# Kernel optimization log

Measured on AMD Instinct MI355X. Metric: run time of the kernel, lower is better.

## Reference

```python
import jax, jax.numpy as jnp
import numpy as np

D_MODEL = 768
N_LAYER = 4
VOCAB = 50257
D_STATE = 16
D_CONV = 4
D_INNER = 2 * D_MODEL
DT_RANK = 48
B, L = 1, 2048


def setup_inputs() -> dict:
    key = jax.random.key(0)
    ks = jax.random.split(key, 12)
    n = lambda k, shape, s=0.02: jax.random.normal(k, shape, dtype=jnp.float32) * s
    return {
        "idx": jax.random.randint(ks[0], (B, L), 0, VOCAB, dtype=jnp.int32),
        "targets": jax.random.randint(ks[1], (B, L), 0, VOCAB, dtype=jnp.int32),
        "embedding": n(ks[2], (VOCAB, D_MODEL)),
        "norm_w": jnp.ones((N_LAYER, D_MODEL), jnp.float32),
        "in_proj_w": n(ks[3], (N_LAYER, 2 * D_INNER, D_MODEL)),
        "conv_w": n(ks[4], (N_LAYER, D_INNER, D_CONV), 0.1),
        "conv_b": jnp.zeros((N_LAYER, D_INNER), jnp.float32),
        "x_proj_w": n(ks[5], (N_LAYER, DT_RANK + 2 * D_STATE, D_INNER)),
        "dt_proj_w": n(ks[6], (N_LAYER, D_INNER, DT_RANK), 0.1),
        # bias so softplus(dt) lands in ~[0.01, 0.1] as in the official init
        "dt_proj_b": jax.random.uniform(ks[7], (N_LAYER, D_INNER), jnp.float32, -4.6, -2.3),
        # A_log = log(1..d_state), the standard S4D-real init
        "A_log": jnp.log(jnp.broadcast_to(jnp.arange(1, D_STATE + 1, dtype=jnp.float32), (N_LAYER, D_INNER, D_STATE))),
        "D_param": jnp.ones((N_LAYER, D_INNER), jnp.float32),
        "out_proj_w": n(ks[8], (N_LAYER, D_MODEL, D_INNER)),
        "norm_f_w": jnp.ones((D_MODEL,), jnp.float32),
    }


def rmsnorm(x, w, eps=1e-5):
    return x * jax.lax.rsqrt(jnp.mean(x * x, -1, keepdims=True) + eps) * w


def causal_conv1d(x, w, b):
    # x: (B,L,d_inner); w: (d_inner, K) depthwise causal conv
    K = w.shape[-1]
    Lx = x.shape[1]
    xp = jnp.pad(x, ((0, 0), (K - 1, 0), (0, 0)))
    y = b
    for k in range(K):
        y = y + xp[:, k:k + Lx, :] * w[:, k]
    return y


def selective_scan(x, dt, A, Bm, Cm, Dp):
    # x, dt: (B,L,d_inner); A: (d_inner,d_state); Bm, Cm: (B,L,d_state)
    bsz, _, d_in = x.shape

    def step(h, inp):
        x_t, dt_t, B_t, C_t = inp  # (B,d_in),(B,d_in),(B,s),(B,s)
        h = jnp.exp(dt_t[:, :, None] * A) * h + (dt_t * x_t)[:, :, None] * B_t[:, None, :]
        return h, jnp.einsum('bds,bs->bd', h, C_t)

    h0 = jnp.zeros((bsz, d_in, A.shape[-1]), x.dtype)
    _, ys = jax.lax.scan(step, h0, (x.swapaxes(0, 1), dt.swapaxes(0, 1), Bm.swapaxes(0, 1), Cm.swapaxes(0, 1)))
    return ys.swapaxes(0, 1) + x * Dp


def mamba_block(x, in_w, cw, cb, xpw, dtw, dtb, a_log, dp, ow):
    xz = x @ in_w.T  # (B,L,2*d_inner)
    xi, z = jnp.split(xz, 2, axis=-1)
    xi = jax.nn.silu(causal_conv1d(xi, cw, cb))
    xdbl = xi @ xpw.T  # (B,L,dt_rank+2*d_state)
    dt = xdbl[..., :DT_RANK]
    Bm = xdbl[..., DT_RANK:DT_RANK + D_STATE]
    Cm = xdbl[..., DT_RANK + D_STATE:]
    dt = jax.nn.softplus(dt @ dtw.T + dtb)
    A = -jnp.exp(a_log)
    y = selective_scan(xi, dt, A, Bm, Cm, dp)
    y = y * jax.nn.silu(z)
    return y @ ow.T


def reference(idx, targets, embedding, norm_w, in_proj_w, conv_w, conv_b, x_proj_w,
              dt_proj_w, dt_proj_b, A_log, D_param, out_proj_w, norm_f_w):
    x = embedding[idx]  # (B,L,D)
    for l in range(N_LAYER):
        x = x + mamba_block(rmsnorm(x, norm_w[l]), in_proj_w[l], conv_w[l], conv_b[l],
                            x_proj_w[l], dt_proj_w[l], dt_proj_b[l], A_log[l],
                            D_param[l], out_proj_w[l])
    x = rmsnorm(x, norm_f_w)
    logits = x @ embedding.T  # tied lm head, (B,L,V)
    # cross_entropy with ignore_index=-1
    logp = jax.nn.log_softmax(logits, axis=-1)
    mask = (targets >= 0).astype(logits.dtype)
    tgt = jnp.clip(targets, 0, VOCAB - 1)
    nll = -jnp.take_along_axis(logp, tgt[..., None], axis=-1)[..., 0]
    loss = jnp.sum(nll * mask) / jnp.maximum(jnp.sum(mask), 1.0)
    return (logits, loss)
```

## Files before the change

### kernel.cpp

```cpp
#include <hip/hip_runtime.h>
#include <stdint.h>


#define D_MODEL 768
#define N_LAYER 4
#define VOCAB 50257
#define D_STATE 16
#define D_INNER 1536
#define DT_RANK 48
#define LSEQ 2048
#define TCHUNK 64
#define NCHUNK 32

#define EMB_E 39321600L
#define W1E 2359296L
#define W2E 196608L
#define W3E 98304L
#define W4E 1179648L
#define PERL (W1E + W2E + W3E + W4E)
#define TOTCVT (EMB_E + 4 * PERL)

typedef unsigned short u16;
typedef __attribute__((ext_vector_type(8))) short short8;
typedef __attribute__((ext_vector_type(4))) float f32x4;

__device__ __forceinline__ u16 f2bf(float f) {
  unsigned int x = __float_as_uint(f);
  x += 0x7fffu + ((x >> 16) & 1u);
  return (u16)(x >> 16);
}
__device__ __forceinline__ float bf2f(u16 v) {
  return __uint_as_float(((unsigned int)v) << 16);
}
__device__ __forceinline__ void gl16(const void* g, void* l) {
  __builtin_amdgcn_global_load_lds((const __attribute__((address_space(1))) void*)g,
                                   (__attribute__((address_space(3))) void*)l, 16, 0, 0);
}

#define PIPELINE(NT)                                                          \
  STAGE(0, 0);                                                                \
  STAGE(32, 1);                                                               \
  {                                                                           \
    int cur = 0;                                                              \
    for (int t = 0; t < (NT); t++) {                                          \
      if (t + 1 < (NT)) { asm volatile("s_waitcnt vmcnt(4)" ::: "memory"); }  \
      else              { asm volatile("s_waitcnt vmcnt(0)" ::: "memory"); }  \
      asm volatile("s_barrier" ::: "memory");                                 \
      short8 af[4], bfr[4];                                                   \
      _Pragma("unroll")                                                       \
      for (int i = 0; i < 4; i++)                                             \
        af[i] = *(const short8*)(&lA[cur][(wm + i * 16 + fr) * 32 + kh]);     \
      _Pragma("unroll")                                                       \
      for (int j = 0; j < 4; j++)                                             \
        bfr[j] = *(const short8*)(&lB[cur][(wn + j * 16 + fr) * 32 + kh]);    \
      asm volatile("s_waitcnt lgkmcnt(0)" ::: "memory");                      \
      asm volatile("s_barrier" ::: "memory");                                 \
      if (t + 2 < (NT)) STAGE((t + 2) * 32, cur);                             \
      _Pragma("unroll")                                                       \
      for (int i = 0; i < 4; i++)                                             \
        _Pragma("unroll")                                                     \
        for (int j = 0; j < 4; j++)                                           \
          acc[i][j] = __builtin_amdgcn_mfma_f32_16x16x32_bf16(af[i], bfr[j],  \
                                                              acc[i][j], 0, 0, 0); \
      cur ^= 1;                                                               \
    }                                                                         \
  }

__global__ void k_convert_all(const float* __restrict__ emb, const float* __restrict__ in_w,
                              const float* __restrict__ xp_w, const float* __restrict__ dt_w,
                              const float* __restrict__ out_w, u16* __restrict__ dst) {
  long i = (long)blockIdx.x * 256 + threadIdx.x;
  float v;
  if (i < EMB_E) {
    long n = i / D_MODEL, k = i % D_MODEL;
    v = (n < VOCAB) ? emb[n * D_MODEL + k] : 0.0f;
  } else {
    long j = i - EMB_E;
    int l = (int)(j / PERL);
    long m = j % PERL;
    if (m < W1E) {
      v = in_w[(long)l * W1E + m];
    } else if (m < W1E + W2E) {
      long mm = m - W1E;
      long n = mm / D_INNER, k = mm % D_INNER;
      v = (n < 80) ? xp_w[(long)l * 80 * D_INNER + n * D_INNER + k] : 0.0f;
    } else if (m < W1E + W2E + W3E) {
      long mm = m - (W1E + W2E);
      long n = mm / 64, k = mm % 64;
      v = (k < DT_RANK) ? dt_w[(long)l * D_INNER * DT_RANK + n * DT_RANK + k] : 0.0f;
    } else {
      long mm = m - (W1E + W2E + W3E);
      v = out_w[(long)l * W4E + mm];
    }
  }
  dst[i] = f2bf(v);
}

__global__ void k_embed_rms(const int* __restrict__ idx, const float* __restrict__ emb,
                            const float* __restrict__ w, float* __restrict__ x,
                            u16* __restrict__ xnb) {
  int t = blockIdx.x, tid = threadIdx.x;
  __shared__ float red[256];
  const float* src = emb + (long)idx[t] * D_MODEL;
  float g[3];
  float s = 0.0f;
#pragma unroll
  for (int q = 0; q < 3; q++) {
    g[q] = src[tid + q * 256];
    s += g[q] * g[q];
  }
  red[tid] = s; __syncthreads();
  for (int o = 128; o > 0; o >>= 1) { if (tid < o) red[tid] += red[tid + o]; __syncthreads(); }
  float scale = rsqrtf(red[0] / (float)D_MODEL + 1e-5f);
#pragma unroll
  for (int q = 0; q < 3; q++) {
    int c = tid + q * 256;
    x[(long)t * D_MODEL + c] = g[q];
    xnb[(long)t * D_MODEL + c] = f2bf(g[q] * scale * w[c]);
  }
}

__global__ void k_rms_red(const float* __restrict__ part, const float* __restrict__ w,
                          float* __restrict__ x, u16* __restrict__ xnb) {
  int t = blockIdx.x, tid = threadIdx.x;
  __shared__ float red[256];
  float g[3];
  float s = 0.0f;
#pragma unroll
  for (int q = 0; q < 3; q++) {
    int c = tid + q * 256;
    long off = (long)t * D_MODEL + c;
    float v = x[off];
#pragma unroll
    for (int p = 0; p < 4; p++) v += part[(size_t)p * LSEQ * D_MODEL + off];
    g[q] = v;
    s += v * v;
  }
  red[tid] = s; __syncthreads();
  for (int o = 128; o > 0; o >>= 1) { if (tid < o) red[tid] += red[tid + o]; __syncthreads(); }
  float scale = rsqrtf(red[0] / (float)D_MODEL + 1e-5f);
#pragma unroll
  for (int q = 0; q < 3; q++) {
    int c = tid + q * 256;
    x[(long)t * D_MODEL + c] = g[q];
    xnb[(long)t * D_MODEL + c] = f2bf(g[q] * scale * w[c]);
  }
}

template<int EPI>
__global__ __launch_bounds__(256) void k_gemm2(
    const u16* __restrict__ A, const u16* __restrict__ W, void* __restrict__ Cv,
    const float* __restrict__ bias, int N, int K, int lda, int ldb, int ldc) {
  __shared__ u16 lA[2][128 * 32];
  __shared__ u16 lB[2][128 * 32];
  const int gx = gridDim.x, gy = gridDim.y;
  int id = blockIdx.x + gx * blockIdx.y;
  int q8 = (gx * gy) >> 3;
  int v = (id & 7) * q8 + (id >> 3);
  const int bx = v / gy, by = v % gy;
  const int brow = by * 128, bcol = bx * 128;
  const int tid = threadIdx.x, wid = tid >> 6, lane = tid & 63;
  const int wm = (wid >> 1) * 64, wn = (wid & 1) * 64;
  const int fr = lane & 15, fq = lane >> 4;
  const int kh = 8 * (fq ^ ((fr >> 1) & 3));
  const int srow = tid >> 2;
  const int lcol = (tid & 3) * 8;
  const int scol = 8 * ((tid & 3) ^ ((srow >> 1) & 3));
  const u16* ga0 = A + (size_t)(brow + srow) * lda + scol;
  const u16* ga1 = A + (size_t)(brow + srow + 64) * lda + scol;
  const u16* gb0 = W + (size_t)(bcol + srow) * ldb + scol;
  const u16* gb1 = W + (size_t)(bcol + srow + 64) * ldb + scol;
  const int lo = srow * 32 + lcol;

  f32x4 acc[4][4];
#pragma unroll
  for (int i = 0; i < 4; i++)
#pragma unroll
    for (int j = 0; j < 4; j++)
#pragma unroll
      for (int r = 0; r < 4; r++) acc[i][j][r] = 0.0f;

  auto STAGE = [&](int k0, int b) {
    gl16(ga0 + k0, &lA[b][lo]);
    gl16(ga1 + k0, &lA[b][lo + 2048]);
    gl16(gb0 + k0, &lB[b][lo]);
    gl16(gb1 + k0, &lB[b][lo + 2048]);
  };

  PIPELINE(K / 32);

#pragma unroll
  for (int i = 0; i < 4; i++)
#pragma unroll
    for (int j = 0; j < 4; j++) {
      int col = bcol + wn + j * 16 + fr;
      if (col < N) {
#pragma unroll
        for (int r = 0; r < 4; r++) {
          int row = brow + wm + i * 16 + fq * 4 + r;
          float val = acc[i][j][r];
          if (EPI == 1) {
            val += bias[col];
            val = (val > 20.0f) ? val : log1pf(__expf(val));
            ((float*)Cv)[(size_t)row * ldc + col] = val;
          } else {
            ((u16*)Cv)[(size_t)row * ldc + col] = f2bf(val);
          }
        }
      }
    }
}

__global__ __launch_bounds__(256) void k_gemm_part(
    const u16* __restrict__ A, const u16* __restrict__ W, float* __restrict__ Cp,
    int N, int Ks, int lda, int ldb, int ldc) {
  __shared__ u16 lA[2][128 * 32];
  __shared__ u16 lB[2][128 * 32];
  const int gx = gridDim.x, gy = gridDim.y;
  int id = blockIdx.x + gx * blockIdx.y;
  int q8 = (gx * gy) >> 3;
  int v = (id & 7) * q8 + (id >> 3);
  const int bx = v / gy, by = v % gy;
  const int brow = by * 128, bcol = bx * 128;
  const int koff = blockIdx.z * Ks;
  const int tid = threadIdx.x, wid = tid >> 6, lane = tid & 63;
  const int wm = (wid >> 1) * 64, wn = (wid & 1) * 64;
  const int fr = lane & 15, fq = lane >> 4;
  const int kh = 8 * (fq ^ ((fr >> 1) & 3));
  const int srow = tid >> 2;
  const int lcol = (tid & 3) * 8;
  const int scol = 8 * ((tid & 3) ^ ((srow >> 1) & 3));
  const u16* ga0 = A + (size_t)(brow + srow) * lda + koff + scol;
  const u16* ga1 = A + (size_t)(brow + srow + 64) * lda + koff + scol;
  const u16* gb0 = W + (size_t)(bcol + srow) * ldb + koff + scol;
  const u16* gb1 = W + (size_t)(bcol + srow + 64) * ldb + koff + scol;
  const int lo = srow * 32 + lcol;

  f32x4 acc[4][4];
#pragma unroll
  for (int i = 0; i < 4; i++)
#pragma unroll
    for (int j = 0; j < 4; j++)
#pragma unroll
      for (int r = 0; r < 4; r++) acc[i][j][r] = 0.0f;

  auto STAGE = [&](int k0, int b) {
    gl16(ga0 + k0, &lA[b][lo]);
    gl16(ga1 + k0, &lA[b][lo + 2048]);
    gl16(gb0 + k0, &lB[b][lo]);
    gl16(gb1 + k0, &lB[b][lo + 2048]);
  };

  PIPELINE(Ks / 32);

  float* Cz = Cp + (size_t)blockIdx.z * LSEQ * ldc;
#pragma unroll
  for (int i = 0; i < 4; i++)
#pragma unroll
    for (int j = 0; j < 4; j++) {
      int col = bcol + wn + j * 16 + fr;
      if (col < N) {
#pragma unroll
        for (int r = 0; r < 4; r++) {
          int row = brow + wm + i * 16 + fq * 4 + r;
          Cz[(size_t)row * ldc + col] = acc[i][j][r];
        }
      }
    }
}

__global__ __launch_bounds__(256, 2) void k_gemm_logits(
    const u16* __restrict__ A, const u16* __restrict__ W, float* __restrict__ C,
    float* __restrict__ part) {
  __shared__ u16 lA[2][256 * 32];
  __shared__ u16 lB[2][128 * 32];
  const int b = blockIdx.x;
  const int xcd = b & 7, slot = b >> 3;
  const int ct = xcd * 50 + (slot >> 3), rt = slot & 7;
  const int brow = rt * 256, bcol = ct * 128;
  const int tid = threadIdx.x, wid = tid >> 6, lane = tid & 63;
  const int wm = (wid >> 1) * 128, wn = (wid & 1) * 64;
  const int fr = lane & 15, fq = lane >> 4;
  const int kh = 8 * (fq ^ ((fr >> 1) & 3));
  const int srow = tid >> 2;
  const int lcol = (tid & 3) * 8;
  const int scol = 8 * ((tid & 3) ^ ((srow >> 1) & 3));
  const u16* ga = A + (size_t)(brow + srow) * D_MODEL + scol;
  const u16* gb = W + (size_t)(bcol + srow) * D_MODEL + scol;
  const int lo = srow * 32 + lcol;

  f32x4 acc[8][4];
#pragma unroll
  for (int i = 0; i < 8; i++)
#pragma unroll
    for (int j = 0; j < 4; j++)
#pragma unroll
      for (int r = 0; r < 4; r++) acc[i][j][r] = 0.0f;

  auto STAGE = [&](int k0, int bb) {
    gl16(ga + k0, &lA[bb][lo]);
    gl16(ga + (size_t)64 * D_MODEL + k0, &lA[bb][lo + 2048]);
    gl16(ga + (size_t)128 * D_MODEL + k0, &lA[bb][lo + 4096]);
    gl16(ga + (size_t)192 * D_MODEL + k0, &lA[bb][lo + 6144]);
    gl16(gb + k0, &lB[bb][lo]);
    gl16(gb + (size_t)64 * D_MODEL + k0, &lB[bb][lo + 2048]);
  };

  STAGE(0, 0);
  STAGE(32, 1);
  int cur = 0;
  const int NT = D_MODEL / 32;
  for (int t = 0; t < NT; t++) {
    if (t + 1 < NT) { asm volatile("s_waitcnt vmcnt(6)" ::: "memory"); }
    else            { asm volatile("s_waitcnt vmcnt(0)" ::: "memory"); }
    asm volatile("s_barrier" ::: "memory");
    short8 af[8], bfr[4];
#pragma unroll
    for (int i = 0; i < 8; i++)
      af[i] = *(const short8*)(&lA[cur][(wm + i * 16 + fr) * 32 + kh]);
#pragma unroll
    for (int j = 0; j < 4; j++)
      bfr[j] = *(const short8*)(&lB[cur][(wn + j * 16 + fr) * 32 + kh]);
    asm volatile("s_waitcnt lgkmcnt(0)" ::: "memory");
    asm volatile("s_barrier" ::: "memory");
    if (t + 2 < NT) STAGE((t + 2) * 32, cur);
    __builtin_amdgcn_s_setprio(1);
#pragma unroll
    for (int i = 0; i < 8; i++)
#pragma unroll
      for (int j = 0; j < 4; j++)
        acc[i][j] = __builtin_amdgcn_mfma_f32_16x16x32_bf16(af[i], bfr[j], acc[i][j], 0, 0, 0);
    __builtin_amdgcn_s_setprio(0);
    cur ^= 1;
  }

  float rs[32];
#pragma unroll
  for (int q = 0; q < 32; q++) rs[q] = 0.0f;
#pragma unroll
  for (int i = 0; i < 8; i++)
#pragma unroll
    for (int j = 0; j < 4; j++) {
      int col = bcol + wn + j * 16 + fr;
      if (col < VOCAB) {
#pragma unroll
        for (int r = 0; r < 4; r++) {
          int row = brow + wm + i * 16 + fq * 4 + r;
          float val = acc[i][j][r];
          C[(size_t)row * VOCAB + col] = val;
          rs[i * 4 + r] += __expf(val - 20.0f);
        }
      }
    }
#pragma unroll
  for (int q = 0; q < 32; q++) {
    float s = rs[q];
    s += __shfl_xor(s, 1); s += __shfl_xor(s, 2);
    s += __shfl_xor(s, 4); s += __shfl_xor(s, 8);
    rs[q] = s;
  }
  if (fr == 0) {
    int pc = ct * 2 + (wn >> 6);
#pragma unroll
    for (int i = 0; i < 8; i++)
#pragma unroll
      for (int r = 0; r < 4; r++) {
        int row = brow + wm + i * 16 + fq * 4 + r;
        part[(size_t)pc * LSEQ + row] = rs[i * 4 + r];
      }
  }
}

__global__ void k_conv_silu(const u16* __restrict__ xzb, const float* __restrict__ cw,
                            const float* __restrict__ cb, u16* __restrict__ xib) {
  int i = blockIdx.x * 256 + threadIdx.x;
  int t = i / (D_INNER / 8), d8 = (i % (D_INNER / 8)) * 8;
  float acc[8];
#pragma unroll
  for (int q = 0; q < 8; q++) acc[q] = cb[d8 + q];
#pragma unroll
  for (int k = 0; k < 4; k++) {
    int tt = t - 3 + k;
    if (tt >= 0) {
      short8 v = *(const short8*)(xzb + (long)tt * (2 * D_INNER) + d8);
#pragma unroll
      for (int q = 0; q < 8; q++) acc[q] += bf2f((u16)v[q]) * cw[(d8 + q) * 4 + k];
    }
  }
  short8 o;
#pragma unroll
  for (int q = 0; q < 8; q++) {
    float s = acc[q] / (1.0f + __expf(-acc[q]));
    o[q] = (short)f2bf(s);
  }
  *(short8*)(xib + (long)t * D_INNER + d8) = o;
}

__global__ void k_red_xd(const float* __restrict__ pxp, float* __restrict__ xdbl,
                         u16* __restrict__ dtp) {
  int i = blockIdx.x * 256 + threadIdx.x;
  int t = i >> 7, k = i & 127;
  if (k < 80) {
    float s = 0.0f;
#pragma unroll
    for (int p = 0; p < 8; p++) s += pxp[(size_t)p * LSEQ * 80 + (long)t * 80 + k];
    xdbl[(long)t * 80 + k] = s;
    if (k < DT_RANK) dtp[(long)t * 64 + k] = f2bf(s);
    else if (k < 64) dtp[(long)t * 64 + k] = 0;
  }
}

__global__ void k_scanA(const float* __restrict__ dt, const u16* __restrict__ xi,
                        const float* __restrict__ xdbl, const float* __restrict__ a_log,
                        float* __restrict__ aprod, float* __restrict__ hend) {
  int d = blockIdx.x * 256 + threadIdx.x;
  int c = blockIdx.y;
  float A[16], ap[16], h[16];
#pragma unroll
  for (int s = 0; s < 16; s++) { A[s] = -__expf(a_log[d * 16 + s]); ap[s] = 1.0f; h[s] = 0.0f; }
  int t0 = c * TCHUNK;
  for (int t = t0; t < t0 + TCHUNK; t++) {
    float dtv = dt[(long)t * D_INNER + d], xv = bf2f(xi[(long)t * D_INNER + d]);
    float dx = dtv * xv;
    const float* Bp = xdbl + (long)t * 80 + DT_RANK;
#pragma unroll
    for (int s = 0; s < 16; s++) {
      float a = __expf(dtv * A[s]);
      h[s] = a * h[s] + dx * Bp[s];
      ap[s] *= a;
    }
  }
  long base = ((long)c * D_INNER + d) * 16;
#pragma unroll
  for (int s = 0; s < 16; s++) { aprod[base + s] = ap[s]; hend[base + s] = h[s]; }
}

__global__ void k_scanB(const float* __restrict__ aprod, const float* __restrict__ hend,
                        float* __restrict__ hinit) {
  int i = blockIdx.x * 256 + threadIdx.x;
  float h = 0.0f;
  for (int c = 0; c < NCHUNK; c++) {
    long idx = (long)c * D_INNER * 16 + i;
    hinit[idx] = h;
    h = aprod[idx] * h + hend[idx];
  }
}

__global__ void k_scanC(const float* __restrict__ dt, const u16* __restrict__ xi,
                        const float* __restrict__ xdbl, const float* __restrict__ a_log,
                        const float* __restrict__ hinit, const float* __restrict__ Dp,
                        const u16* __restrict__ xzb, u16* __restrict__ yb) {
  int d = blockIdx.x * 256 + threadIdx.x;
  int c = blockIdx.y;
  float A[16], h[16];
  long hb = (long)c * D_INNER * 16 + (long)d * 16;
#pragma unroll
  for (int s = 0; s < 16; s++) { A[s] = -__expf(a_log[d * 16 + s]); h[s] = hinit[hb + s]; }
  float Dv = Dp[d];
  int t0 = c * TCHUNK;
  for (int t = t0; t < t0 + TCHUNK; t++) {
    float dtv = dt[(long)t * D_INNER + d], xv = bf2f(xi[(long)t * D_INNER + d]);
    float dx = dtv * xv;
    const float* Bp = xdbl + (long)t * 80 + DT_RANK;
    const float* Cp = Bp + D_STATE;
    float o = xv * Dv;
#pragma unroll
    for (int s = 0; s < 16; s++) {
      float a = __expf(dtv * A[s]);
      h[s] = a * h[s] + dx * Bp[s];
      o += h[s] * Cp[s];
    }
    float z = bf2f(xzb[(long)t * (2 * D_INNER) + D_INNER + d]);
    yb[(long)t * D_INNER + d] = f2bf(o * (z / (1.0f + __expf(-z))));
  }
}

__global__ void k_lse_final(const float* __restrict__ part, const float* __restrict__ logits,
                            const int* __restrict__ tgt, float* __restrict__ nll,
                            float* __restrict__ msk) {
  int t = blockIdx.x * 256 + threadIdx.x;
  float s = 0.0f;
  for (int p = 0; p < 800; p++) s += part[(size_t)p * LSEQ + t];
  float lse = 20.0f + __logf(s);
  int tg = tgt[t];
  float mk = tg >= 0 ? 1.0f : 0.0f;
  int tc = tg < 0 ? 0 : (tg > VOCAB - 1 ? VOCAB - 1 : tg);
  nll[t] = (lse - logits[(size_t)t * VOCAB + tc]) * mk;
  msk[t] = mk;
}

__global__ void k_loss(const float* __restrict__ nll, const float* __restrict__ msk,
                       float* __restrict__ out) {
  int tid = threadIdx.x;
  __shared__ float r1[256], r2[256];
  float a = 0.0f, b = 0.0f;
  for (int i = tid; i < LSEQ; i += 256) { a += nll[i]; b += msk[i]; }
  r1[tid] = a; r2[tid] = b; __syncthreads();
  for (int o = 128; o > 0; o >>= 1) {
    if (tid < o) { r1[tid] += r1[tid + o]; r2[tid] += r2[tid + o]; }
    __syncthreads();
  }
  if (tid == 0) out[0] = r1[0] / fmaxf(r2[0], 1.0f);
}

extern "C" void kernel_launch(void* const* d_in, const int* in_sizes, int n_in,
                              void* d_out, int out_size, void* d_ws, size_t ws_size,
                              hipStream_t stream) {
  const int*   idx    = (const int*)d_in[0];
  const int*   tgt    = (const int*)d_in[1];
  const float* emb    = (const float*)d_in[2];
  const float* norm_w = (const float*)d_in[3];
  const float* in_w   = (const float*)d_in[4];
  const float* conv_w = (const float*)d_in[5];
  const float* conv_b = (const float*)d_in[6];
  const float* xp_w   = (const float*)d_in[7];
  const float* dt_w   = (const float*)d_in[8];
  const float* dt_b   = (const float*)d_in[9];
  const float* a_log  = (const float*)d_in[10];
  const float* d_par  = (const float*)d_in[11];
  const float* out_w  = (const float*)d_in[12];
  const float* normf  = (const float*)d_in[13];

  float* logits = (float*)d_out;
  float* loss   = logits + (size_t)LSEQ * VOCAB;

  char* base = (char*)d_ws;
  size_t off = 0;
  auto alloc = [&](size_t bytes) -> char* {
    char* r = base + off;
    off = (off + bytes + 255) & ~(size_t)255;
    return r;
  };
  u16*   wcat = (u16*)  alloc((size_t)TOTCVT * 2);
  float* x    = (float*)alloc((size_t)LSEQ * D_MODEL * 4);
  u16*   xnb  = (u16*)  alloc((size_t)LSEQ * D_MODEL * 2);
  u16*   xzb  = (u16*)  alloc((size_t)LSEQ * 2 * D_INNER * 2);
  u16*   xib  = (u16*)  alloc((size_t)LSEQ * D_INNER * 2);
  float* xdbl = (float*)alloc((size_t)LSEQ * 80 * 4);
  u16*   dtp  = (u16*)  alloc((size_t)LSEQ * 64 * 2);
  float* dtl  = (float*)alloc((size_t)LSEQ * D_INNER * 4);
  u16*   yb   = (u16*)  alloc((size_t)LSEQ * D_INNER * 2);
  float* pxp  = (float*)alloc((size_t)8 * LSEQ * 80 * 4);
  float* pop  = (float*)alloc((size_t)4 * LSEQ * D_MODEL * 4);
  float* apr  = (float*)alloc((size_t)NCHUNK * D_INNER * 16 * 4);
  float* hen  = (float*)alloc((size_t)NCHUNK * D_INNER * 16 * 4);
  float* hin  = (float*)alloc((size_t)NCHUNK * D_INNER * 16 * 4);
  float* nll  = (float*)alloc((size_t)LSEQ * 4);
  float* msk  = (float*)alloc((size_t)LSEQ * 4);
  float* part = pop;
  (void)ws_size; (void)in_sizes; (void)n_in; (void)out_size;

  const u16* embb = wcat;

  k_convert_all<<<(unsigned)(TOTCVT / 256), 256, 0, stream>>>(emb, in_w, xp_w, dt_w, out_w, wcat);
  k_embed_rms<<<LSEQ, 256, 0, stream>>>(idx, emb, norm_w, x, xnb);

  for (int l = 0; l < N_LAYER; l++) {
    const u16* w1 = wcat + EMB_E + (long)l * PERL;
    const u16* w2 = w1 + W1E;
    const u16* w3 = w2 + W2E;
    const u16* w4 = w3 + W3E;

    k_gemm2<2><<<dim3(24, 16), 256, 0, stream>>>(
        xnb, w1, xzb, nullptr, 2 * D_INNER, D_MODEL, D_MODEL, D_MODEL, 2 * D_INNER);

    k_conv_silu<<<(LSEQ * D_INNER / 8) / 256, 256, 0, stream>>>(
        xzb, conv_w + (long)l * D_INNER * 4, conv_b + l * D_INNER, xib);

    k_gemm_part<<<dim3(1, 16, 8), 256, 0, stream>>>(
        xib, w2, pxp, 80, D_INNER / 8, D_INNER, D_INNER, 80);
    k_red_xd<<<(LSEQ * 128) / 256, 256, 0, stream>>>(pxp, xdbl, dtp);

    k_gemm2<1><<<dim3(12, 16), 256, 0, stream>>>(
        dtp, w3, dtl, dt_b + l * D_INNER, D_INNER, 64, 64, 64, D_INNER);

    const float* al = a_log + (long)l * D_INNER * D_STATE;
    k_scanA<<<dim3(D_INNER / 256, NCHUNK), 256, 0, stream>>>(dtl, xib, xdbl, al, apr, hen);
    k_scanB<<<(D_INNER * 16) / 256, 256, 0, stream>>>(apr, hen, hin);
    k_scanC<<<dim3(D_INNER / 256, NCHUNK), 256, 0, stream>>>(
        dtl, xib, xdbl, al, hin, d_par + l * D_INNER, xzb, yb);

    k_gemm_part<<<dim3(6, 16, 4), 256, 0, stream>>>(
        yb, w4, pop, D_MODEL, D_INNER / 4, D_INNER, D_INNER, D_MODEL);

    const float* wn = (l < N_LAYER - 1) ? (norm_w + (l + 1) * D_MODEL) : normf;
    k_rms_red<<<LSEQ, 256, 0, stream>>>(pop, wn, x, xnb);
  }

  k_gemm_logits<<<400 * 8, 256, 0, stream>>>(xnb, embb, logits, part);
  k_lse_final<<<LSEQ / 256, 256, 0, stream>>>(part, logits, tgt, nll, msk);
  k_loss<<<1, 256, 0, stream>>>(nll, msk, loss);
}
```

Measured before the change: 1.171 ms.

## Triple-buffer GEMM pipelines, vectorize weight conversion, and retune split-K and logits occupancy

Deepens the GEMM shared-memory pipeline from two to three stages and raises wave priority around the MFMA block, so more loads are in flight and compute is favoured over issue. The bf16 weight conversion kernel now handles four elements per thread with a vector store. The x_proj split-K factor doubles to 16, logits stores become nontemporal, and the logits kernel's launch bounds now request 3 blocks per SM instead of 2. Partial-sum buffers are merged into one pool. The extra LDS per GEMM block and the tighter register budget for logits may reduce occupancy or cause spills.

```diff
diff --git a/kernel.cpp b/kernel.cpp
--- a/kernel.cpp
+++ b/kernel.cpp
@@ -23,6 +23,7 @@
 typedef unsigned short u16;
 typedef __attribute__((ext_vector_type(8))) short short8;
 typedef __attribute__((ext_vector_type(4))) float f32x4;
+typedef __attribute__((ext_vector_type(4))) unsigned short us4;
 
 __device__ __forceinline__ u16 f2bf(float f) {
   unsigned int x = __float_as_uint(f);
@@ -37,14 +38,17 @@
                                    (__attribute__((address_space(3))) void*)l, 16, 0, 0);
 }
 
-#define PIPELINE(NT)                                                          \
+#define PIPELINE3(NT)                                                         \
   STAGE(0, 0);                                                                \
-  STAGE(32, 1);                                                               \
+  if ((NT) > 1) STAGE(32, 1);                                                 \
+  if ((NT) > 2) STAGE(64, 2);                                                 \
   {                                                                           \
     int cur = 0;                                                              \
     for (int t = 0; t < (NT); t++) {                                          \
-      if (t + 1 < (NT)) { asm volatile("s_waitcnt vmcnt(4)" ::: "memory"); }  \
-      else              { asm volatile("s_waitcnt vmcnt(0)" ::: "memory"); }  \
+      int rem = (NT) - 1 - t;                                                 \
+      if (rem >= 2)      { asm volatile("s_waitcnt vmcnt(8)" ::: "memory"); } \
+      else if (rem == 1) { asm volatile("s_waitcnt vmcnt(4)" ::: "memory"); } \
+      else               { asm volatile("s_waitcnt vmcnt(0)" ::: "memory"); } \
       asm volatile("s_barrier" ::: "memory");                                 \
       short8 af[4], bfr[4];                                                   \
       _Pragma("unroll")                                                       \
@@ -55,45 +59,54 @@
         bfr[j] = *(const short8*)(&lB[cur][(wn + j * 16 + fr) * 32 + kh]);    \
       asm volatile("s_waitcnt lgkmcnt(0)" ::: "memory");                      \
       asm volatile("s_barrier" ::: "memory");                                 \
-      if (t + 2 < (NT)) STAGE((t + 2) * 32, cur);                             \
+      if (t + 3 < (NT)) STAGE((t + 3) * 32, cur);                             \
+      __builtin_amdgcn_s_setprio(1);                                          \
       _Pragma("unroll")                                                       \
       for (int i = 0; i < 4; i++)                                             \
         _Pragma("unroll")                                                     \
         for (int j = 0; j < 4; j++)                                           \
           acc[i][j] = __builtin_amdgcn_mfma_f32_16x16x32_bf16(af[i], bfr[j],  \
                                                               acc[i][j], 0, 0, 0); \
-      cur ^= 1;                                                               \
+      __builtin_amdgcn_s_setprio(0);                                          \
+      cur = (cur == 2) ? 0 : cur + 1;                                         \
     }                                                                         \
   }
 
 __global__ void k_convert_all(const float* __restrict__ emb, const float* __restrict__ in_w,
                               const float* __restrict__ xp_w, const float* __restrict__ dt_w,
                               const float* __restrict__ out_w, u16* __restrict__ dst) {
-  long i = (long)blockIdx.x * 256 + threadIdx.x;
-  float v;
-  if (i < EMB_E) {
-    long n = i / D_MODEL, k = i % D_MODEL;
-    v = (n < VOCAB) ? emb[n * D_MODEL + k] : 0.0f;
-  } else {
-    long j = i - EMB_E;
-    int l = (int)(j / PERL);
-    long m = j % PERL;
-    if (m < W1E) {
-      v = in_w[(long)l * W1E + m];
-    } else if (m < W1E + W2E) {
-      long mm = m - W1E;
-      long n = mm / D_INNER, k = mm % D_INNER;
-      v = (n < 80) ? xp_w[(long)l * 80 * D_INNER + n * D_INNER + k] : 0.0f;
-    } else if (m < W1E + W2E + W3E) {
-      long mm = m - (W1E + W2E);
-      long n = mm / 64, k = mm % 64;
-      v = (k < DT_RANK) ? dt_w[(long)l * D_INNER * DT_RANK + n * DT_RANK + k] : 0.0f;
+  long i0 = ((long)blockIdx.x * 256 + threadIdx.x) * 4;
+  if (i0 >= TOTCVT) return;
+  us4 o;
+#pragma unroll
+  for (int q = 0; q < 4; q++) {
+    long i = i0 + q;
+    float v;
+    if (i < EMB_E) {
+      long n = i / D_MODEL, k = i % D_MODEL;
+      v = (n < VOCAB) ? emb[n * D_MODEL + k] : 0.0f;
     } else {
-      long mm = m - (W1E + W2E + W3E);
-      v = out_w[(long)l * W4E + mm];
+      long j = i - EMB_E;
+      int l = (int)(j / PERL);
+      long m = j % PERL;
+      if (m < W1E) {
+        v = in_w[(long)l * W1E + m];
+      } else if (m < W1E + W2E) {
+        long mm = m - W1E;
+        long n = mm / D_INNER, k = mm % D_INNER;
+        v = (n < 80) ? xp_w[(long)l * 80 * D_INNER + n * D_INNER + k] : 0.0f;
+      } else if (m < W1E + W2E + W3E) {
+        long mm = m - (W1E + W2E);
+        long n = mm / 64, k = mm % 64;
+        v = (k < DT_RANK) ? dt_w[(long)l * D_INNER * DT_RANK + n * DT_RANK + k] : 0.0f;
+      } else {
+        long mm = m - (W1E + W2E + W3E);
+        v = out_w[(long)l * W4E + mm];
+      }
     }
-  }
-  dst[i] = f2bf(v);
+    o[q] = f2bf(v);
+  }
+  *(us4*)(dst + i0) = o;
 }
 
 __global__ void k_embed_rms(const int* __restrict__ idx, const float* __restrict__ emb,
@@ -151,8 +164,8 @@
 __global__ __launch_bounds__(256) void k_gemm2(
     const u16* __restrict__ A, const u16* __restrict__ W, void* __restrict__ Cv,
     const float* __restrict__ bias, int N, int K, int lda, int ldb, int ldc) {
-  __shared__ u16 lA[2][128 * 32];
-  __shared__ u16 lB[2][128 * 32];
+  __shared__ u16 lA[3][128 * 32];
+  __shared__ u16 lB[3][128 * 32];
   const int gx = gridDim.x, gy = gridDim.y;
   int id = blockIdx.x + gx * blockIdx.y;
   int q8 = (gx * gy) >> 3;
@@ -187,7 +200,7 @@
     gl16(gb1 + k0, &lB[b][lo + 2048]);
   };
 
-  PIPELINE(K / 32);
+  PIPELINE3(K / 32);
 
 #pragma unroll
   for (int i = 0; i < 4; i++)
@@ -214,8 +227,8 @@
 __global__ __launch_bounds__(256) void k_gemm_part(
     const u16* __restrict__ A, const u16* __restrict__ W, float* __restrict__ Cp,
     int N, int Ks, int lda, int ldb, int ldc) {
-  __shared__ u16 lA[2][128 * 32];
-  __shared__ u16 lB[2][128 * 32];
+  __shared__ u16 lA[3][128 * 32];
+  __shared__ u16 lB[3][128 * 32];
   const int gx = gridDim.x, gy = gridDim.y;
   int id = blockIdx.x + gx * blockIdx.y;
   int q8 = (gx * gy) >> 3;
@@ -251,7 +264,7 @@
     gl16(gb1 + k0, &lB[b][lo + 2048]);
   };
 
-  PIPELINE(Ks / 32);
+  PIPELINE3(Ks / 32);
 
   float* Cz = Cp + (size_t)blockIdx.z * LSEQ * ldc;
 #pragma unroll
@@ -269,7 +282,7 @@
     }
 }
 
-__global__ __launch_bounds__(256, 2) void k_gemm_logits(
+__global__ __launch_bounds__(256, 3) void k_gemm_logits(
     const u16* __restrict__ A, const u16* __restrict__ W, float* __restrict__ C,
     float* __restrict__ part) {
   __shared__ u16 lA[2][256 * 32];
@@ -347,7 +360,7 @@
         for (int r = 0; r < 4; r++) {
           int row = brow + wm + i * 16 + fq * 4 + r;
           float val = acc[i][j][r];
-          C[(size_t)row * VOCAB + col] = val;
+          __builtin_nontemporal_store(val, &C[(size_t)row * VOCAB + col]);
           rs[i * 4 + r] += __expf(val - 20.0f);
         }
       }
@@ -403,7 +416,7 @@
   if (k < 80) {
     float s = 0.0f;
 #pragma unroll
-    for (int p = 0; p < 8; p++) s += pxp[(size_t)p * LSEQ * 80 + (long)t * 80 + k];
+    for (int p = 0; p < 16; p++) s += pxp[(size_t)p * LSEQ * 80 + (long)t * 80 + k];
     xdbl[(long)t * 80 + k] = s;
     if (k < DT_RANK) dtp[(long)t * 64 + k] = f2bf(s);
     else if (k < 64) dtp[(long)t * 64 + k] = 0;
@@ -540,19 +553,21 @@
   u16*   dtp  = (u16*)  alloc((size_t)LSEQ * 64 * 2);
   float* dtl  = (float*)alloc((size_t)LSEQ * D_INNER * 4);
   u16*   yb   = (u16*)  alloc((size_t)LSEQ * D_INNER * 2);
-  float* pxp  = (float*)alloc((size_t)8 * LSEQ * 80 * 4);
-  float* pop  = (float*)alloc((size_t)4 * LSEQ * D_MODEL * 4);
+  float* pool = (float*)alloc((size_t)4 * LSEQ * D_MODEL * 4);
   float* apr  = (float*)alloc((size_t)NCHUNK * D_INNER * 16 * 4);
   float* hen  = (float*)alloc((size_t)NCHUNK * D_INNER * 16 * 4);
   float* hin  = (float*)alloc((size_t)NCHUNK * D_INNER * 16 * 4);
   float* nll  = (float*)alloc((size_t)LSEQ * 4);
   float* msk  = (float*)alloc((size_t)LSEQ * 4);
-  float* part = pop;
+  float* pxp  = pool;
+  float* pop  = pool;
+  float* part = pool;
   (void)ws_size; (void)in_sizes; (void)n_in; (void)out_size;
 
   const u16* embb = wcat;
 
-  k_convert_all<<<(unsigned)(TOTCVT / 256), 256, 0, stream>>>(emb, in_w, xp_w, dt_w, out_w, wcat);
+  k_convert_all<<<(unsigned)((TOTCVT / 4 + 255) / 256), 256, 0, stream>>>(
+      emb, in_w, xp_w, dt_w, out_w, wcat);
   k_embed_rms<<<LSEQ, 256, 0, stream>>>(idx, emb, norm_w, x, xnb);
 
   for (int l = 0; l < N_LAYER; l++) {
@@ -567,8 +582,8 @@
     k_conv_silu<<<(LSEQ * D_INNER / 8) / 256, 256, 0, stream>>>(
         xzb, conv_w + (long)l * D_INNER * 4, conv_b + l * D_INNER, xib);
 
-    k_gemm_part<<<dim3(1, 16, 8), 256, 0, stream>>>(
-        xib, w2, pxp, 80, D_INNER / 8, D_INNER, D_INNER, 80);
+    k_gemm_part<<<dim3(1, 16, 16), 256, 0, stream>>>(
+        xib, w2, pxp, 80, D_INNER / 16, D_INNER, D_INNER, 80);
     k_red_xd<<<(LSEQ * 128) / 256, 256, 0, stream>>>(pxp, xdbl, dtp);
 
     k_gemm2<1><<<dim3(12, 16), 256, 0, stream>>>(
```

New measurement: 1.698 ms. 1.45x slower.
